# Optimization experiments

Measured on AMD Instinct MI355X. Metric: run time of the kernel, lower is better.

Reference implementation:

```python
import jax, jax.numpy as jnp
import numpy as np

MOMENTUM = 0.1  # matches init_kwargs


def _amp_norm(x, running_amp, momentum):
    # x: [B, C, H, W] real; running_amp: [C, H, W]
    fft = jnp.fft.fft2(x, axes=(-2, -1))            # [B,C,H,W] complex64
    amp = jnp.abs(fft)                               # amplitude spectrum
    pha = jnp.angle(fft)                             # phase spectrum
    amp_mean = amp.mean(axis=0)                      # batch-averaged amplitude [C,H,W]
    # First call (buffer all-zero): adopt batch amplitude; otherwise EMA update.
    new_amp = jnp.where(jnp.sum(running_amp) == 0,
                        amp_mean,
                        (1.0 - momentum) * running_amp + momentum * amp_mean)
    # Rebuild spectrum with shared (running) amplitude and per-sample phase.
    fft_new = new_amp[None].astype(jnp.complex64) * jnp.exp(1j * pha)
    x_out = jnp.real(jnp.fft.ifft2(fft_new, axes=(-2, -1))).astype(x.dtype)
    return x_out, new_amp


def setup_inputs() -> dict:
    key = jax.random.key(0)
    x = jax.random.normal(key, (32, 3, 384, 384), dtype=jnp.float32)
    running_amp = jnp.zeros((3, 384, 384), dtype=jnp.float32)
    return {"x": x, "running_amp": running_amp}


def reference(x, running_amp):
    x_out, _ = _amp_norm(x, running_amp, MOMENTUM)
    return x_out
```

## Files before the change

### kernel.cpp

```cpp
#include <hip/hip_runtime.h>
#include <hip/hip_fp16.h>
#include <math.h>


#define NFFT   384
#define NW     193
#define PLANE  147456
#define IMGS   96
#define LSTRB  389
#define TSTR   33

__device__ __forceinline__ float2 cmul(float2 a, float2 b) {
    return make_float2(a.x*b.x - a.y*b.y, a.x*b.y + a.y*b.x);
}
__device__ __forceinline__ float2 cadd(float2 a, float2 b) { return make_float2(a.x+b.x, a.y+b.y); }
__device__ __forceinline__ float2 csub(float2 a, float2 b) { return make_float2(a.x-b.x, a.y-b.y); }

template<int DIR>
__device__ __forceinline__ void fft12(float2 z[12]) {
    const float dir = (float)DIR;
    const float H = 0.86602540378443864676f;
    float2 G[12];
    #pragma unroll
    for (int b = 0; b < 3; ++b) {
        float2 a0 = z[b], a1 = z[b+3], a2 = z[b+6], a3 = z[b+9];
        float2 t0 = cadd(a0, a2), t1 = csub(a0, a2);
        float2 t2 = cadd(a1, a3), t3 = csub(a1, a3);
        G[b*4+0] = cadd(t0, t2);
        G[b*4+1] = make_float2(t1.x + dir*t3.y, t1.y - dir*t3.x);
        G[b*4+2] = csub(t0, t2);
        G[b*4+3] = make_float2(t1.x - dir*t3.y, t1.y + dir*t3.x);
    }
    const float2 W1 = make_float2( H,    -dir*0.5f);
    const float2 W2 = make_float2( 0.5f, -dir*H);
    const float2 W3 = make_float2( 0.0f, -dir);
    const float2 W4 = make_float2(-0.5f, -dir*H);
    const float2 W6 = make_float2(-1.0f,  0.0f);
    G[4+1] = cmul(G[4+1], W1);  G[4+2] = cmul(G[4+2], W2);  G[4+3] = cmul(G[4+3], W3);
    G[8+1] = cmul(G[8+1], W2);  G[8+2] = cmul(G[8+2], W4);  G[8+3] = cmul(G[8+3], W6);
    const float b3 = -dir * H;
    #pragma unroll
    for (int ka = 0; ka < 4; ++ka) {
        float2 g0 = G[ka], g1 = G[4+ka], g2 = G[8+ka];
        float2 t = cadd(g1, g2), d = csub(g1, g2);
        float2 u = make_float2(g0.x - 0.5f*t.x, g0.y - 0.5f*t.y);
        z[ka]   = cadd(g0, t);
        z[ka+4] = make_float2(u.x - b3*d.y, u.y + b3*d.x);
        z[ka+8] = make_float2(u.x + b3*d.y, u.y - b3*d.x);
    }
}

struct Tw32 { float2 w16, w8, w4, w2; float s16, s8, s4, s2, s1; };

template<int DIR>
__device__ __forceinline__ float2 stage_w(int l, int m) {
    if (l & m) {
        float ph = 3.14159265358979323846f * (float)(l & (m-1)) / (float)m;
        float sv, cv; sincosf(ph, &sv, &cv);
        return make_float2(cv, -(float)DIR * sv);
    }
    return make_float2(1.0f, 0.0f);
}

template<int DIR>
__device__ __forceinline__ Tw32 make_tw32(int l) {
    Tw32 T;
    T.w16 = stage_w<DIR>(l, 16);
    T.w8  = stage_w<DIR>(l, 8);
    T.w4  = stage_w<DIR>(l, 4);
    T.w2  = (l & 2) ? ((l & 1) ? make_float2(0.0f, -(float)DIR) : make_float2(1.0f, 0.0f))
                    : make_float2(1.0f, 0.0f);
    T.s16 = (l & 16) ? -1.0f : 1.0f;
    T.s8  = (l & 8)  ? -1.0f : 1.0f;
    T.s4  = (l & 4)  ? -1.0f : 1.0f;
    T.s2  = (l & 2)  ? -1.0f : 1.0f;
    T.s1  = (l & 1)  ? -1.0f : 1.0f;
    return T;
}

__device__ __forceinline__ float2 bfly(float2 v, int mask, float s, float2 w) {
    float2 p, t;
    p.x = __shfl_xor(v.x, mask, 64);
    p.y = __shfl_xor(v.y, mask, 64);
    t.x = fmaf(s, v.x, p.x);
    t.y = fmaf(s, v.y, p.y);
    return cmul(t, w);
}

__device__ __forceinline__ float2 fft32_slot(float2 v, const Tw32& T) {
    v = bfly(v, 16, T.s16, T.w16);
    v = bfly(v, 8,  T.s8,  T.w8);
    v = bfly(v, 4,  T.s4,  T.w4);
    v = bfly(v, 2,  T.s2,  T.w2);
    float2 p;
    p.x = __shfl_xor(v.x, 1, 64);
    p.y = __shfl_xor(v.y, 1, 64);
    v.x = fmaf(T.s1, v.x, p.x);
    v.y = fmaf(T.s1, v.y, p.y);
    return v;
}

template<int DIR>
__device__ __forceinline__ void fft384_reg(float2 z[12], int l) {
    fft12<DIR>(z);
    float ang = (6.28318530717958647692f / 384.0f) * (float)l;
    float sv, cv; sincosf(ang, &sv, &cv);
    float2 w1 = make_float2(cv, -(float)DIR * sv);
    float2 wk = w1;
    z[1] = cmul(z[1], wk);
    #pragma unroll
    for (int k = 2; k < 12; ++k) { wk = cmul(wk, w1); z[k] = cmul(z[k], wk); }
    Tw32 T = make_tw32<DIR>(l);
    #pragma unroll
    for (int k = 0; k < 12; ++k) z[k] = fft32_slot(z[k], T);
}

__global__ __launch_bounds__(256, 3) void k_fft_rows_fwd(const float* __restrict__ x,
                                                         __half2* __restrict__ At) {
    __shared__ float2 lbuf[16 * LSTRB];
    int tid = threadIdx.x, grp = tid >> 5, l = tid & 31;
    int img = blockIdx.x / 12, g = blockIdx.x % 12;
    const float* xi = x + (size_t)img * PLANE + (size_t)g * 32 * NFFT;
    #pragma unroll
    for (int pp = 0; pp < 2; ++pp) {
        int p = grp + 8 * pp;
        const float* xa = xi + (size_t)(2 * p) * NFFT;
        const float* xb = xa + NFFT;
        float2 z[12];
        #pragma unroll
        for (int j = 0; j < 12; ++j) z[j] = make_float2(xa[32*j + l], xb[32*j + l]);
        fft384_reg<1>(z, l);
        int r = __brev((unsigned)l) >> 27;
        float2* s = lbuf + p * LSTRB;
        #pragma unroll
        for (int k = 0; k < 12; ++k) s[k + 12*r] = z[k];
    }
    __syncthreads();
    int h0 = g * 32;
    int q = l >> 1, odd = l & 1;
    #pragma unroll
    for (int pass = 0; pass < 13; ++pass) {
        #pragma unroll
        for (int ww = 0; ww < 2; ++ww) {
            int w = pass * 16 + grp * 2 + ww;
            if (w <= 192) {
                float2 Z  = lbuf[q * LSTRB + w];
                float2 Zm = lbuf[q * LSTRB + (w == 0 ? 0 : NFFT - w)];
                float2 v;
                if (odd) v = make_float2( 0.5f * (Z.y + Zm.y), -0.5f * (Z.x - Zm.x));
                else     v = make_float2( 0.5f * (Z.x + Zm.x),  0.5f * (Z.y - Zm.y));
                At[((size_t)img * NW + w) * NFFT + h0 + l] = __floats2half2_rn(v.x, v.y);
            }
        }
    }
}

__global__ __launch_bounds__(256, 8) void k_fft_cols_fwd(__half2* __restrict__ At) {
    int tid = threadIdx.x, grp = tid >> 5, l = tid & 31;
    int img = blockIdx.x / 25, cg = blockIdx.x % 25;
    int w = cg * 8 + grp;
    if (w > 192) return;
    __half2* col = At + ((size_t)img * NW + w) * NFFT;
    float2 z[12];
    #pragma unroll
    for (int j = 0; j < 12; ++j) z[j] = __half22float2(col[32*j + l]);
    fft384_reg<1>(z, l);
    int r = __brev((unsigned)l) >> 27;
    #pragma unroll
    for (int k = 0; k < 12; ++k)
        col[k + 12*r] = __floats2half2_rn(z[k].x, z[k].y);
}

__global__ __launch_bounds__(256) void k_flag(const float* __restrict__ r,
                                              float* __restrict__ flag) {
    __shared__ float sm[256];
    int t = blockIdx.x * 1024 + threadIdx.x * 4;
    float4 v = *(const float4*)(r + t);
    sm[threadIdx.x] = v.x + v.y + v.z + v.w;
    __syncthreads();
    for (int s = 128; s > 0; s >>= 1) {
        if (threadIdx.x < s) sm[threadIdx.x] += sm[threadIdx.x + s];
        __syncthreads();
    }
    if (threadIdx.x == 0) atomicAdd(flag, sm[0]);
}

__global__ __launch_bounds__(384) void k_amp(const __half2* __restrict__ At,
                                             float* __restrict__ ampm) {
    int c = blockIdx.x / NW;
    int w = blockIdx.x - c * NW;
    int h = threadIdx.x;
    const __half2* base = At + (size_t)w * NFFT + h;
    float s = 0.0f;
    #pragma unroll 4
    for (int b = 0; b < 32; ++b) {
        float2 z = __half22float2(base[(size_t)(b * 3 + c) * (NW * NFFT)]);
        s += sqrtf(z.x * z.x + z.y * z.y);
    }
    ampm[((size_t)c * NW + w) * NFFT + h] = s * (1.0f / 32.0f);
}

__global__ __launch_bounds__(256, 8) void k_ifft_cols_scale(__half2* __restrict__ At,
                                                            const float* __restrict__ ampm,
                                                            const float* __restrict__ running,
                                                            const float* __restrict__ flag) {
    int tid = threadIdx.x, grp = tid >> 5, l = tid & 31;
    int img = blockIdx.x / 25, cg = blockIdx.x % 25;
    int w = cg * 8 + grp;
    if (w > 192) return;
    int c = img % 3;
    bool adopt = (flag[0] == 0.0f);
    const float inv = 1.0f / (float)NFFT;
    __half2*     col = At + ((size_t)img * NW + w) * NFFT;
    const float* ac  = ampm + ((size_t)c * NW + w) * NFFT;
    float2 z[12];
    #pragma unroll
    for (int j = 0; j < 12; ++j) {
        int n = 32*j + l;
        float2 zv = __half22float2(col[n]);
        float am = ac[n];
        float na;
        if (adopt) na = am;
        else na = 0.9f * running[((size_t)c * NFFT + n) * NFFT + w] + 0.1f * am;
        float mag = sqrtf(zv.x*zv.x + zv.y*zv.y);
        if (mag > 0.0f) { float sc = na / mag; z[j] = make_float2(zv.x*sc, zv.y*sc); }
        else            { z[j] = make_float2(na, 0.0f); }
    }
    fft384_reg<-1>(z, l);
    int r = __brev((unsigned)l) >> 27;
    #pragma unroll
    for (int k = 0; k < 12; ++k)
        col[k + 12*r] = __floats2half2_rn(z[k].x * inv, z[k].y * inv);
}

__global__ __launch_bounds__(256, 5) void k_ifft_rows_out(const __half2* __restrict__ At,
                                                          float* __restrict__ out) {
    __shared__ __half2 tile[NW * TSTR];
    int tid = threadIdx.x, grp = tid >> 5, l = tid & 31;
    int img = blockIdx.x / 12, g = blockIdx.x % 12;
    int h0 = g * 32;
    #pragma unroll
    for (int i = 0; i < 25; ++i) {
        int idx = i * 256 + tid;
        if (idx < NW * 32) {
            int w = idx >> 5, hh = idx & 31;
            tile[w * TSTR + hh] = At[((size_t)img * NW + w) * NFFT + h0 + hh];
        }
    }
    __syncthreads();
    const float inv = 1.0f / (float)NFFT;
    #pragma unroll
    for (int pp = 0; pp < 2; ++pp) {
        int q = grp + 8 * pp;
        float2 z[12];
        #pragma unroll
        for (int j = 0; j < 12; ++j) {
            int n = 32*j + l;
            if (n <= 192) {
                float2 Fa = __half22float2(tile[n * TSTR + 2*q]);
                float2 Fb = __half22float2(tile[n * TSTR + 2*q + 1]);
                z[j] = make_float2(Fa.x - Fb.y, Fa.y + Fb.x);
            } else {
                int m2 = NFFT - n;
                float2 Fa = __half22float2(tile[m2 * TSTR + 2*q]);
                float2 Fb = __half22float2(tile[m2 * TSTR + 2*q + 1]);
                z[j] = make_float2(Fa.x + Fb.y, Fb.x - Fa.y);
            }
        }
        fft384_reg<-1>(z, l);
        int r = __brev((unsigned)l) >> 27;
        float* oa = out + (size_t)img * PLANE + (size_t)(h0 + 2*q) * NFFT;
        float* ob = oa + NFFT;
        #pragma unroll
        for (int k = 0; k < 12; ++k) {
            int n = k + 12*r;
            oa[n] = z[k].x * inv;
            ob[n] = z[k].y * inv;
        }
    }
}

extern "C" void kernel_launch(void* const* d_in, const int* in_sizes, int n_in,
                              void* d_out, int out_size, void* d_ws, size_t ws_size,
                              hipStream_t stream) {
    const float* x       = (const float*)d_in[0];
    const float* running = (const float*)d_in[1];
    float* out = (float*)d_out;

    char* ws = (char*)d_ws;
    __half2* At   = (__half2*)ws;
    float*   ampm = (float*)(ws + 28459008);
    float*   flag = (float*)(ws + 28459008 + 889344);

    hipMemsetAsync(flag, 0, 4, stream);
    k_flag<<<432, 256, 0, stream>>>(running, flag);
    k_fft_rows_fwd<<<IMGS * 12, 256, 0, stream>>>(x, At);
    k_fft_cols_fwd<<<IMGS * 25, 256, 0, stream>>>(At);
    k_amp<<<3 * NW, 384, 0, stream>>>(At, ampm);
    k_ifft_cols_scale<<<IMGS * 25, 256, 0, stream>>>(At, ampm, running, flag);
    k_ifft_rows_out<<<IMGS * 12, 256, 0, stream>>>(At, out);
}
```

Measured before the change: 226.7 us.

## Use decimation-in-time inverse FFTs to make column and output stores coalesced

```diff
diff --git a/kernel.cpp b/kernel.cpp
--- a/kernel.cpp
+++ b/kernel.cpp
@@ -115,6 +115,63 @@
     for (int k = 0; k < 12; ++k) z[k] = fft32_slot(z[k], T);
 }
 
+struct TwD { float2 w2, w4, w8, w16; };
+
+template<int DIR>
+__device__ __forceinline__ float2 dit_stage_w(int l, int mask) {
+    float ph = 3.14159265358979323846f * (float)(l & (mask-1)) / (float)mask;
+    float sv, cv; sincosf(ph, &sv, &cv);
+    return make_float2(cv, -(float)DIR * sv);
+}
+
+template<int DIR>
+__device__ __forceinline__ TwD make_twd(int l) {
+    TwD T;
+    T.w2  = (l & 1) ? make_float2(0.0f, -(float)DIR) : make_float2(1.0f, 0.0f);
+    T.w4  = dit_stage_w<DIR>(l, 4);
+    T.w8  = dit_stage_w<DIR>(l, 8);
+    T.w16 = dit_stage_w<DIR>(l, 16);
+    return T;
+}
+
+__device__ __forceinline__ float2 dit_bfly(float2 v, int mask, int hi, float2 w) {
+    float2 b = hi ? cmul(w, v) : v;
+    float2 p;
+    p.x = __shfl_xor(b.x, mask, 64);
+    p.y = __shfl_xor(b.y, mask, 64);
+    float s = hi ? -1.0f : 1.0f;
+    return make_float2(fmaf(s, b.x, p.x), fmaf(s, b.y, p.y));
+}
+
+__device__ __forceinline__ float2 dit32_slot(float2 v, const TwD& T, int l) {
+    {
+        float2 p;
+        p.x = __shfl_xor(v.x, 1, 64);
+        p.y = __shfl_xor(v.y, 1, 64);
+        float s = (l & 1) ? -1.0f : 1.0f;
+        v = make_float2(fmaf(s, v.x, p.x), fmaf(s, v.y, p.y));
+    }
+    v = dit_bfly(v, 2,  l & 2,  T.w2);
+    v = dit_bfly(v, 4,  l & 4,  T.w4);
+    v = dit_bfly(v, 8,  l & 8,  T.w8);
+    v = dit_bfly(v, 16, l & 16, T.w16);
+    return v;
+}
+
+__device__ __forceinline__ void ifft384_dit(float2 zk[12], int l) {
+    TwD T = make_twd<-1>(l);
+    #pragma unroll
+    for (int k = 0; k < 12; ++k) zk[k] = dit32_slot(zk[k], T, l);
+    float ang = (6.28318530717958647692f / 384.0f) * (float)l;
+    float sv, cv; sincosf(ang, &sv, &cv);
+    float2 w1 = make_float2(cv, sv);
+    float2 wk = w1;
+    zk[1] = cmul(zk[1], wk);
+    #pragma unroll
+    for (int k = 2; k < 12; ++k) { wk = cmul(wk, w1); zk[k] = cmul(zk[k], wk); }
+    fft12<-1>(zk);
+}
+
 __global__ __launch_bounds__(256, 3) void k_fft_rows_fwd(const float* __restrict__ x,
                                                          __half2* __restrict__ At) {
     __shared__ float2 lbuf[16 * LSTRB];
@@ -165,10 +222,9 @@
     #pragma unroll
     for (int j = 0; j < 12; ++j) z[j] = __half22float2(col[32*j + l]);
     fft384_reg<1>(z, l);
-    int r = __brev((unsigned)l) >> 27;
     #pragma unroll
     for (int k = 0; k < 12; ++k)
-        col[k + 12*r] = __floats2half2_rn(z[k].x, z[k].y);
+        col[k * 32 + l] = __floats2half2_rn(z[k].x, z[k].y);
 }
 
 __global__ __launch_bounds__(256) void k_flag(const float* __restrict__ r,
@@ -210,27 +266,30 @@
     if (w > 192) return;
     int c = img % 3;
     bool adopt = (flag[0] == 0.0f);
+    int br = __brev((unsigned)l) >> 27;
     const float inv = 1.0f / (float)NFFT;
     __half2*     col = At + ((size_t)img * NW + w) * NFFT;
     const float* ac  = ampm + ((size_t)c * NW + w) * NFFT;
-    float2 z[12];
-    #pragma unroll
-    for (int j = 0; j < 12; ++j) {
-        int n = 32*j + l;
-        float2 zv = __half22float2(col[n]);
-        float am = ac[n];
+    float2 zk[12];
+    #pragma unroll
+    for (int k = 0; k < 12; ++k) {
+        int pos = k * 32 + l;
+        float2 zv = __half22float2(col[pos]);
+        float am = ac[pos];
         float na;
         if (adopt) na = am;
-        else na = 0.9f * running[((size_t)c * NFFT + n) * NFFT + w] + 0.1f * am;
+        else {
+            int n = k + 12 * br;
+            na = 0.9f * running[((size_t)c * NFFT + n) * NFFT + w] + 0.1f * am;
+        }
         float mag = sqrtf(zv.x*zv.x + zv.y*zv.y);
-        if (mag > 0.0f) { float sc = na / mag; z[j] = make_float2(zv.x*sc, zv.y*sc); }
-        else            { z[j] = make_float2(na, 0.0f); }
-    }
-    fft384_reg<-1>(z, l);
-    int r = __brev((unsigned)l) >> 27;
-    #pragma unroll
-    for (int k = 0; k < 12; ++k)
-        col[k + 12*r] = __floats2half2_rn(z[k].x * inv, z[k].y * inv);
+        if (mag > 0.0f) { float sc = na / mag; zk[k] = make_float2(zv.x*sc, zv.y*sc); }
+        else            { zk[k] = make_float2(na, 0.0f); }
+    }
+    ifft384_dit(zk, l);
+    #pragma unroll
+    for (int j = 0; j < 12; ++j)
+        col[32 * j + l] = __floats2half2_rn(zk[j].x * inv, zk[j].y * inv);
 }
 
 __global__ __launch_bounds__(256, 5) void k_ifft_rows_out(const __half2* __restrict__ At,
@@ -249,33 +308,33 @@
     }
     __syncthreads();
     const float inv = 1.0f / (float)NFFT;
+    int br = __brev((unsigned)l) >> 27;
     #pragma unroll
     for (int pp = 0; pp < 2; ++pp) {
         int q = grp + 8 * pp;
-        float2 z[12];
-        #pragma unroll
-        for (int j = 0; j < 12; ++j) {
-            int n = 32*j + l;
+        float2 zk[12];
+        #pragma unroll
+        for (int k = 0; k < 12; ++k) {
+            int n = k + 12 * br;
             if (n <= 192) {
                 float2 Fa = __half22float2(tile[n * TSTR + 2*q]);
                 float2 Fb = __half22float2(tile[n * TSTR + 2*q + 1]);
-                z[j] = make_float2(Fa.x - Fb.y, Fa.y + Fb.x);
+                zk[k] = make_float2(Fa.x - Fb.y, Fa.y + Fb.x);
             } else {
                 int m2 = NFFT - n;
                 float2 Fa = __half22float2(tile[m2 * TSTR + 2*q]);
                 float2 Fb = __half22float2(tile[m2 * TSTR + 2*q + 1]);
-                z[j] = make_float2(Fa.x + Fb.y, Fb.x - Fa.y);
+                zk[k] = make_float2(Fa.x + Fb.y, Fb.x - Fa.y);
             }
         }
-        fft384_reg<-1>(z, l);
-        int r = __brev((unsigned)l) >> 27;
+        ifft384_dit(zk, l);
         float* oa = out + (size_t)img * PLANE + (size_t)(h0 + 2*q) * NFFT;
         float* ob = oa + NFFT;
         #pragma unroll
-        for (int k = 0; k < 12; ++k) {
-            int n = k + 12*r;
-            oa[n] = z[k].x * inv;
-            ob[n] = z[k].y * inv;
+        for (int j = 0; j < 12; ++j) {
+            int n = 32 * j + l;
+            oa[n] = zk[j].x * inv;
+            ob[n] = zk[j].y * inv;
         }
     }
 }
```

Measured after the change: 212.0 us. -6.5%, faster.
